# Performance work log

Measured on AMD Instinct MI355X. Metric: run time of the kernel, lower is better.

Reference implementation:

```python
import jax, jax.numpy as jnp
import numpy as np

# Problem sizes: batch B, n variables, m constraints (dense nnz pattern)
B, N, M = 256, 128, 192
# OSQP ADMM parameters (scaling=0, fixed rho; OSQP defaults)
RHO = 0.1      # step size
SIGMA = 1e-6   # regularization
ALPHA = 1.6    # relaxation
N_ITERS = 400  # fixed iteration count (jit-friendly surrogate for max_iter/tolerances)


def setup_inputs() -> dict:
    key = jax.random.key(0)
    k1, k2, k3, k4, k5, k6 = jax.random.split(key, 6)
    G = jax.random.normal(k1, (B, N, N), dtype=jnp.float32)
    # PSD quadratic cost: P = G G^T / n + 0.5 I
    P_val = jnp.einsum('bij,bkj->bik', G, G) / N + 0.5 * jnp.eye(N, dtype=jnp.float32)
    q_val = jax.random.normal(k2, (B, N), dtype=jnp.float32)
    A_val = jax.random.normal(k3, (B, M, N), dtype=jnp.float32) / jnp.sqrt(jnp.float32(N))
    # Bounds bracketing a feasible point x0 so every QP is solvable
    x0 = jax.random.normal(k4, (B, N), dtype=jnp.float32)
    z0 = jnp.einsum('bmn,bn->bm', A_val, x0)
    l_val = z0 - jnp.abs(jax.random.normal(k5, (B, M), dtype=jnp.float32)) - 0.1
    u_val = z0 + jnp.abs(jax.random.normal(k6, (B, M), dtype=jnp.float32)) + 0.1
    return {'P_val': P_val, 'q_val': q_val, 'A_val': A_val,
            'l_val': l_val, 'u_val': u_val}


def _osqp_admm(P, q, A, l, u):
    """Batched OSQP ADMM with fixed rho: solves argmin 1/2 x'Px + q'x s.t. l<=Ax<=u."""
    dt = P.dtype
    I_n = jnp.eye(N, dtype=dt)
    I_m = jnp.eye(M, dtype=dt)
    AT = jnp.swapaxes(A, -1, -2)  # [B, n, m]
    # KKT matrix [[P + sigma*I, A'], [A, -I/rho]]  -> [B, n+m, n+m]
    top = jnp.concatenate([P + SIGMA * I_n, AT], axis=-1)
    bot = jnp.concatenate([A, jnp.broadcast_to(-(1.0 / RHO) * I_m, (P.shape[0], M, M))], axis=-1)
    K = jnp.concatenate([top, bot], axis=-2)
    Kinv = jnp.linalg.inv(K)  # factorize once (rho fixed)

    x0 = jnp.zeros_like(q)
    z0 = jnp.zeros_like(l)
    y0 = jnp.zeros_like(l)

    def step(carry, _):
        x, z, y = carry
        rhs = jnp.concatenate([SIGMA * x - q, z - y / RHO], axis=-1)  # [B, n+m]
        sol = jnp.einsum('bij,bj->bi', Kinv, rhs)
        xt, nu = sol[:, :N], sol[:, N:]
        zt = z + (nu - y) / RHO
        x_new = ALPHA * xt + (1.0 - ALPHA) * x
        zc = ALPHA * zt + (1.0 - ALPHA) * z
        z_new = jnp.clip(zc + y / RHO, l, u)  # projection onto [l, u]
        y_new = y + RHO * (zc - z_new)
        return (x_new, z_new, y_new), None

    (x, z, y), _ = jax.lax.scan(step, (x0, z0, y0), None, length=N_ITERS)
    return x


def reference(P_val, q_val, A_val, l_val, u_val):
    # Returns the batch of primal solutions x_hat, shape [B, n]
    return _osqp_admm(P_val, q_val, A_val, l_val, u_val)
```

## Files before the change

kernel.cpp:

```cpp
#include <hip/hip_runtime.h>


#define Nn 128
#define Mm 192
constexpr float RHO_    = 0.1f;
constexpr float RHOINV_ = 10.0f;
constexpr float SIGMA_  = 1e-6f;
constexpr float ALPHA_  = 1.6f;
constexpr int   NITERS_ = 400;

typedef float v2f __attribute__((ext_vector_type(2)));
typedef float v4f __attribute__((ext_vector_type(4)));

template<int CTRL>
__device__ __forceinline__ float dpp_add(float x) {
  int y = __builtin_amdgcn_update_dpp(__float_as_int(x), __float_as_int(x),
                                      CTRL, 0xF, 0xF, false);
  return x + __int_as_float(y);
}
__device__ __forceinline__ float red16(float x) {
  x = dpp_add<0x121>(x); x = dpp_add<0x122>(x);
  x = dpp_add<0x124>(x); x = dpp_add<0x128>(x);
  return x;
}

template<int K0>
__device__ __forceinline__ void gj_block(float rr[32], float* __restrict__ buf0,
                                         float* __restrict__ buf1,
                                         const int irow, const int qq) {
  const bool qsel = (qq == K0);
  #pragma unroll
  for (int kk = 0; kk < 32; kk++) {
    const int k = 32*K0 + kk;
    float* wb = ((kk & 1) == 0) ? buf0 : buf1;
    if (irow == k) {
      #pragma unroll
      for (int j4 = 0; j4 < 8; j4++)
        *(float4*)&wb[36*qq + 4*j4] = *(const float4*)&rr[4*j4];
    }
    __syncthreads();
    const float akk  = wb[36*K0 + kk];
    float pinv = __builtin_amdgcn_rcpf(akk);
    pinv = pinv + pinv*(1.0f - akk*pinv);
    constexpr int QP = K0 | (K0<<2) | (K0<<4) | (K0<<6);
    const int fi = __builtin_amdgcn_update_dpp(__float_as_int(rr[kk]),
                      __float_as_int(rr[kk]), QP, 0xF, 0xF, false);
    const float f = __int_as_float(fi);
    const bool piv = (irow == k);
    float gfac = f * pinv;
    gfac = piv ? (1.0f - pinv) : gfac;
    float rk[32];
    #pragma unroll
    for (int j4 = 0; j4 < 8; j4++)
      *(float4*)&rk[4*j4] = *(const float4*)&wb[36*qq + 4*j4];
    #pragma unroll
    for (int j = 0; j < 32; j++) rr[j] -= gfac * rk[j];
    const float pivfix = piv ? pinv : -gfac;
    if (qsel) rr[kk] = pivfix;
  }
}

__global__ void __launch_bounds__(512, 2)
precompute_kernel(const float* __restrict__ Pg, const float* __restrict__ qg,
                  const float* __restrict__ Ag, float* __restrict__ wsWt,
                  float* __restrict__ wsC)
{
  __shared__ float smem[16384];
  const int t = threadIdx.x;
  const int b = blockIdx.x;
  const float* __restrict__ Pb = Pg + (size_t)b*Nn*Nn;
  const float* __restrict__ qb = qg + (size_t)b*Nn;
  const float* __restrict__ Ab = Ag + (size_t)b*Mm*Nn;

  {
    const int ar = t & 31;
    const int bc = t >> 5;
    float acc[4][8];
    #pragma unroll
    for (int a=0;a<4;a++)
      #pragma unroll
      for (int j=0;j<8;j++) acc[a][j]=0.f;

    for (int c=0;c<6;c++) {
      __syncthreads();
      {
        const float4* src = (const float4*)(Ab + c*32*Nn);
        float4* dst = (float4*)smem;
        dst[t]     = src[t];
        dst[t+512] = src[t+512];
      }
      __syncthreads();
      #pragma unroll 2
      for (int m=0;m<32;m++) {
        const float4 ra  = *(const float4*)&smem[m*Nn + 4*ar];
        const float4 cb0 = *(const float4*)&smem[m*Nn + 8*bc];
        const float4 cb1 = *(const float4*)&smem[m*Nn + 8*bc + 4];
        const float rv[4] = {ra.x, ra.y, ra.z, ra.w};
        const float cv[8] = {cb0.x,cb0.y,cb0.z,cb0.w,cb1.x,cb1.y,cb1.z,cb1.w};
        #pragma unroll
        for (int a=0;a<4;a++)
          #pragma unroll
          for (int j=0;j<8;j++) acc[a][j] += rv[a]*cv[j];
      }
    }
    __syncthreads();
    #pragma unroll
    for (int a=0;a<4;a++) {
      const int i = 4*ar + a;
      #pragma unroll
      for (int j=0;j<8;j++) {
        const int jj = 8*bc + j;
        float v = Pb[i*Nn + jj] + RHO_*acc[a][j];
        if (i == jj) v += SIGMA_;
        smem[i*Nn + jj] = v;
      }
    }
    __syncthreads();
  }

  {
    const int irow = t >> 2;
    const int qq   = t & 3;
    float rr[32];
    #pragma unroll
    for (int j=0;j<32;j++) rr[j] = smem[irow*Nn + 32*qq + j];
    __syncthreads();
    float* buf0 = smem;
    float* buf1 = smem + 144;
    gj_block<0>(rr, buf0, buf1, irow, qq);
    gj_block<1>(rr, buf0, buf1, irow, qq);
    gj_block<2>(rr, buf0, buf1, irow, qq);
    gj_block<3>(rr, buf0, buf1, irow, qq);
    __syncthreads();
    #pragma unroll
    for (int j=0;j<32;j++) smem[irow*Nn + 32*qq + j] = rr[j];
  }
  __syncthreads();

  {
    const int jr = t & 63, kc = t >> 6;
    v2f acc[3][8];
    #pragma unroll
    for (int a=0;a<3;a++)
      #pragma unroll
      for (int p=0;p<8;p++) acc[a][p] = (v2f){0.f,0.f};

    for (int mi=0; mi<32; mi++) {
      const v4f a0 = *(const v4f*)&Ab[(jr      )*Nn + 4*mi];
      const v4f a1 = *(const v4f*)&Ab[(jr +  64)*Nn + 4*mi];
      const v4f a2 = *(const v4f*)&Ab[(jr + 128)*Nn + 4*mi];
      const float am[3][4] = {{a0.x,a0.y,a0.z,a0.w},
                              {a1.x,a1.y,a1.z,a1.w},
                              {a2.x,a2.y,a2.z,a2.w}};
      #pragma unroll
      for (int q=0;q<4;q++) {
        const int m = 4*mi + q;
        const v4f w0 = *(const v4f*)&smem[m*Nn + 16*kc +  0];
        const v4f w1 = *(const v4f*)&smem[m*Nn + 16*kc +  4];
        const v4f w2 = *(const v4f*)&smem[m*Nn + 16*kc +  8];
        const v4f w3 = *(const v4f*)&smem[m*Nn + 16*kc + 12];
        const v2f wp[8] = {(v2f){w0.x,w0.y},(v2f){w0.z,w0.w},
                           (v2f){w1.x,w1.y},(v2f){w1.z,w1.w},
                           (v2f){w2.x,w2.y},(v2f){w2.z,w2.w},
                           (v2f){w3.x,w3.y},(v2f){w3.z,w3.w}};
        #pragma unroll
        for (int a=0;a<3;a++) {
          const v2f amv = (v2f){am[a][q], am[a][q]};
          #pragma unroll
          for (int p=0;p<8;p++) acc[a][p] += amv * wp[p];
        }
      }
    }
    float* wb = wsWt + (size_t)b*Mm*Nn;
    #pragma unroll
    for (int a=0;a<3;a++) {
      const int j = jr + 64*a;
      #pragma unroll
      for (int x=0;x<4;x++) {
        *(float4*)&wb[j*Nn + 16*kc + 4*x] =
          make_float4(acc[a][2*x].x, acc[a][2*x].y, acc[a][2*x+1].x, acc[a][2*x+1].y);
      }
    }
  }
  if (t < Nn) {
    float cc = 0.f;
    #pragma unroll 4
    for (int k=0;k<Nn;k++) cc += smem[k*Nn + t] * qb[k];
    wsC[(size_t)b*Nn + t] = cc;
  }
}

#define ABASE 0
#define WBASE 6912
__global__ void __launch_bounds__(1024, 4)
loop_kernel(const float* __restrict__ Ag, const float* __restrict__ lg,
            const float* __restrict__ ug, const float* __restrict__ wsWt,
            const float* __restrict__ wsC, float* __restrict__ outg)
{
  __shared__ float smem[13824];
  const int t = threadIdx.x, b = blockIdx.x;
  const int ig = t >> 4, cg = t & 15;
  const float* __restrict__ Ab = Ag   + (size_t)b*Mm*Nn;
  const float* __restrict__ Wb = wsWt + (size_t)b*Mm*Nn;
  const float* __restrict__ cb = wsC  + (size_t)b*Nn;

  const int  pm  = 64*cg + ig;
  const bool isp = (cg < 3);

  float dreg = 0.f, lreg = 0.f, ureg = 0.f;
  if (isp) {
    lreg = lg[(size_t)b*Mm + pm];
    ureg = ug[(size_t)b*Mm + pm];
    const float4* ar = (const float4*)(Ab + pm*Nn);
    const float4* cr = (const float4*)cb;
    #pragma unroll 4
    for (int k4=0;k4<32;k4++) {
      const float4 av = ar[k4], cv = cr[k4];
      dreg += av.x*cv.x + av.y*cv.y + av.z*cv.z + av.w*cv.w;
    }
  }

  v2f accv[3][12];
  #pragma unroll
  for (int a=0;a<3;a++)
    #pragma unroll
    for (int jj=0;jj<12;jj++) accv[a][jj] = (v2f){0.f,0.f};

  for (int kc=0; kc<4; kc++) {
    __syncthreads();
    {
      int x = t;
      {
        const int row = x>>3, c4 = x&7;
        *(float4*)&smem[ABASE + 36*row + 4*c4] = *(const float4*)&Ab[row*Nn + 32*kc + 4*c4];
        *(float4*)&smem[WBASE + 36*row + 4*c4] = *(const float4*)&Wb[row*Nn + 32*kc + 4*c4];
      }
      if (t < 512) {
        x = t + 1024;
        const int row = x>>3, c4 = x&7;
        *(float4*)&smem[ABASE + 36*row + 4*c4] = *(const float4*)&Ab[row*Nn + 32*kc + 4*c4];
        *(float4*)&smem[WBASE + 36*row + 4*c4] = *(const float4*)&Wb[row*Nn + 32*kc + 4*c4];
      }
    }
    __syncthreads();
    #pragma unroll
    for (int m4=0; m4<8; m4++) {
      const v4f a0 = *(const v4f*)&smem[ABASE + 36*(ig      ) + 4*m4];
      const v4f a1 = *(const v4f*)&smem[ABASE + 36*(ig +  64) + 4*m4];
      const v4f a2 = *(const v4f*)&smem[ABASE + 36*(ig + 128) + 4*m4];
      #pragma unroll
      for (int jj=0; jj<12; jj++) {
        const v4f w = *(const v4f*)&smem[WBASE + 36*(cg + 16*jj) + 4*m4];
        const v2f wlo = (v2f){w.x,w.y}, whi = (v2f){w.z,w.w};
        accv[0][jj] += (v2f){a0.x,a0.y}*wlo + (v2f){a0.z,a0.w}*whi;
        accv[1][jj] += (v2f){a1.x,a1.y}*wlo + (v2f){a1.z,a1.w}*whi;
        accv[2][jj] += (v2f){a2.x,a2.y}*wlo + (v2f){a2.z,a2.w}*whi;
      }
    }
  }
  float Vr[3][12];
  #pragma unroll
  for (int a=0;a<3;a++)
    #pragma unroll
    for (int jj=0;jj<12;jj++)
      Vr[a][jj] = accv[a][jj].x + accv[a][jj].y;

  __syncthreads();
  float* sT0  = smem;
  float* sT1  = smem + 192;
  float* sacc = smem + 384;
  if (t < Mm) sT0[t] = 0.f;
  __syncthreads();

  const int woff = (pm & 15)*12 + (pm >> 4);
  float sreg = 0.f, preg = 0.f, Sacc = 0.f;
  const float* sR0 = sT0 + 12*cg;
  const float* sR1 = sT1 + 12*cg;

#define ITER(RD, WR)                                                           \
  {                                                                            \
    const float4 sA = *(const float4*)(RD);                                    \
    const float4 sB = *(const float4*)((RD) + 4);                              \
    const float4 sC = *(const float4*)((RD) + 8);                              \
    float r0 = Vr[0][0]*sA.x + Vr[0][1]*sA.y + Vr[0][2]*sA.z + Vr[0][3]*sA.w   \
             + Vr[0][4]*sB.x + Vr[0][5]*sB.y + Vr[0][6]*sB.z + Vr[0][7]*sB.w   \
             + Vr[0][8]*sC.x + Vr[0][9]*sC.y + Vr[0][10]*sC.z + Vr[0][11]*sC.w;\
    float r1 = Vr[1][0]*sA.x + Vr[1][1]*sA.y + Vr[1][2]*sA.z + Vr[1][3]*sA.w   \
             + Vr[1][4]*sB.x + Vr[1][5]*sB.y + Vr[1][6]*sB.z + Vr[1][7]*sB.w   \
             + Vr[1][8]*sC.x + Vr[1][9]*sC.y + Vr[1][10]*sC.z + Vr[1][11]*sC.w;\
    float r2 = Vr[2][0]*sA.x + Vr[2][1]*sA.y + Vr[2][2]*sA.z + Vr[2][3]*sA.w   \
             + Vr[2][4]*sB.x + Vr[2][5]*sB.y + Vr[2][6]*sB.z + Vr[2][7]*sB.w   \
             + Vr[2][8]*sC.x + Vr[2][9]*sC.y + Vr[2][10]*sC.z + Vr[2][11]*sC.w;\
    r0 = red16(r0); r1 = red16(r1); r2 = red16(r2);                            \
    if (isp) {                                                                 \
      const float r  = (cg==0) ? r0 : ((cg==1) ? r1 : r2);                     \
      const float w  = r - dreg;                                               \
      const float v  = fmaf(ALPHA_, w, preg);                                  \
      const float z  = __builtin_amdgcn_fmed3f(v, lreg, ureg);                 \
      const float sn = RHO_ * fmaf(2.0f, z, -v);                               \
      (WR)[woff] = sn;                                                         \
      Sacc = (1.f-ALPHA_)*Sacc + ALPHA_*sreg;                                  \
      sreg = sn;                                                               \
      preg = fmaf(-ALPHA_, z, v);                                              \
    }                                                                          \
    __syncthreads();                                                           \
  }

  #pragma unroll 1
  for (int it2 = 0; it2 < NITERS_/2; it2++) {
    ITER(sR0, sT1)
    ITER(sR1, sT0)
  }
#undef ITER

  if (isp) sacc[pm] = Sacc;
  __syncthreads();
  if (t < Nn) {
    float acc = -cb[t];
    #pragma unroll 4
    for (int j=0;j<Mm;j++) acc += Wb[j*Nn + t] * sacc[j];
    outg[(size_t)b*Nn + t] = acc;
  }
}

extern "C" void kernel_launch(void* const* d_in, const int* in_sizes, int n_in,
                              void* d_out, int out_size, void* d_ws, size_t ws_size,
                              hipStream_t stream) {
  const float* P = (const float*)d_in[0];
  const float* q = (const float*)d_in[1];
  const float* A = (const float*)d_in[2];
  const float* l = (const float*)d_in[3];
  const float* u = (const float*)d_in[4];
  (void)in_sizes; (void)n_in; (void)out_size; (void)ws_size;
  float* wsWt = (float*)d_ws;
  float* wsC  = wsWt + (size_t)256*Mm*Nn;
  precompute_kernel<<<256, 512, 0, stream>>>(P, q, A, wsWt, wsC);
  loop_kernel<<<256, 1024, 0, stream>>>(A, l, u, wsWt, wsC, (float*)d_out);
}
```

Before: 461.2 us.

## Restructure ADMM loop to one thread per constraint with early exit

The loop kernel drops from 1024 to 256 threads per block. Each constraint thread now keeps its full 192-entry row of the iteration matrix in registers, which removes the 16-lane DPP reductions. W is stored transposed and staged in padded LDS, and the final x reconstruction reads from LDS. A fixed-point check every few iterations breaks out of the loop once the state stops changing bit-exactly, skipping the remaining iterations. The risks are heavy register pressure (192 floats per thread, one wave per EU) and a large dynamic LDS allocation.

After: 670.3 us. 1.45x slower.

```diff
diff --git a/kernel.cpp b/kernel.cpp
--- a/kernel.cpp
+++ b/kernel.cpp
@@ -4,25 +4,12 @@
 #define Nn 128
 #define Mm 192
 constexpr float RHO_    = 0.1f;
-constexpr float RHOINV_ = 10.0f;
 constexpr float SIGMA_  = 1e-6f;
 constexpr float ALPHA_  = 1.6f;
 constexpr int   NITERS_ = 400;
 
 typedef float v2f __attribute__((ext_vector_type(2)));
 typedef float v4f __attribute__((ext_vector_type(4)));
-
-template<int CTRL>
-__device__ __forceinline__ float dpp_add(float x) {
-  int y = __builtin_amdgcn_update_dpp(__float_as_int(x), __float_as_int(x),
-                                      CTRL, 0xF, 0xF, false);
-  return x + __int_as_float(y);
-}
-__device__ __forceinline__ float red16(float x) {
-  x = dpp_add<0x121>(x); x = dpp_add<0x122>(x);
-  x = dpp_add<0x124>(x); x = dpp_add<0x128>(x);
-  return x;
-}
 
 template<int K0>
 __device__ __forceinline__ void gj_block(float rr[32], float* __restrict__ buf0,
@@ -171,14 +158,15 @@
         }
       }
     }
-    float* wb = wsWt + (size_t)b*Mm*Nn;
+    float* wb = wsWt + (size_t)b*Nn*Mm;
     #pragma unroll
     for (int a=0;a<3;a++) {
       const int j = jr + 64*a;
       #pragma unroll
-      for (int x=0;x<4;x++) {
-        *(float4*)&wb[j*Nn + 16*kc + 4*x] =
-          make_float4(acc[a][2*x].x, acc[a][2*x].y, acc[a][2*x+1].x, acc[a][2*x+1].y);
+      for (int p=0;p<8;p++) {
+        const int col = 16*kc + 2*p;
+        wb[(size_t)(col    )*Mm + j] = acc[a][p].x;
+        wb[(size_t)(col + 1)*Mm + j] = acc[a][p].y;
       }
     }
   }
@@ -190,136 +178,134 @@
   }
 }
 
-#define ABASE 0
-#define WBASE 6912
-__global__ void __launch_bounds__(1024, 4)
+#define WT_LD 196
+#define OFF_S0   (Nn*WT_LD)
+#define OFF_S1   (OFF_S0 + Mm)
+#define OFF_SACC (OFF_S1 + Mm)
+#define OFF_C    (OFF_SACC + Mm)
+#define OFF_FLAG (OFF_C + Nn)
+#define LOOP_LDS_FLOATS (OFF_FLAG + 2)
+
+__global__ void __launch_bounds__(256)
+__attribute__((amdgpu_waves_per_eu(1, 1)))
 loop_kernel(const float* __restrict__ Ag, const float* __restrict__ lg,
-            const float* __restrict__ ug, const float* __restrict__ wsWt,
+            const float* __restrict__ ug, const float* __restrict__ wsWtT,
             const float* __restrict__ wsC, float* __restrict__ outg)
 {
-  __shared__ float smem[13824];
+  extern __shared__ float smem[];
   const int t = threadIdx.x, b = blockIdx.x;
-  const int ig = t >> 4, cg = t & 15;
+  const bool act = (t < Mm);
+  const float* __restrict__ Wg = wsWtT + (size_t)b*Nn*Mm;
+  const float* __restrict__ cb = wsC  + (size_t)b*Nn;
   const float* __restrict__ Ab = Ag   + (size_t)b*Mm*Nn;
-  const float* __restrict__ Wb = wsWt + (size_t)b*Mm*Nn;
-  const float* __restrict__ cb = wsC  + (size_t)b*Nn;
-
-  const int  pm  = 64*cg + ig;
-  const bool isp = (cg < 3);
+
+  float* WT    = smem;
+  float* sT0   = smem + OFF_S0;
+  float* sT1   = smem + OFF_S1;
+  float* sacc  = smem + OFF_SACC;
+  float* c_s   = smem + OFF_C;
+  float* sflag = smem + OFF_FLAG;
+
+  if (act) {
+    #pragma unroll 4
+    for (int k = 0; k < Nn; k++) WT[k*WT_LD + t] = Wg[(size_t)k*Mm + t];
+  }
+  if (t < Nn) c_s[t] = cb[t];
+  if (act) sT0[t] = 0.f;
+  if (t < 2) sflag[t] = 0.f;
+  __syncthreads();
 
   float dreg = 0.f, lreg = 0.f, ureg = 0.f;
-  if (isp) {
-    lreg = lg[(size_t)b*Mm + pm];
-    ureg = ug[(size_t)b*Mm + pm];
-    const float4* ar = (const float4*)(Ab + pm*Nn);
-    const float4* cr = (const float4*)cb;
+  v2f Vrow[96];
+  if (act) {
+    lreg = lg[(size_t)b*Mm + t];
+    ureg = ug[(size_t)b*Mm + t];
+    const float4* ar = (const float4*)(Ab + (size_t)t*Nn);
+    const float4* cr = (const float4*)c_s;
     #pragma unroll 4
-    for (int k4=0;k4<32;k4++) {
+    for (int k4 = 0; k4 < 32; k4++) {
       const float4 av = ar[k4], cv = cr[k4];
       dreg += av.x*cv.x + av.y*cv.y + av.z*cv.z + av.w*cv.w;
     }
-  }
-
-  v2f accv[3][12];
-  #pragma unroll
-  for (int a=0;a<3;a++)
-    #pragma unroll
-    for (int jj=0;jj<12;jj++) accv[a][jj] = (v2f){0.f,0.f};
-
-  for (int kc=0; kc<4; kc++) {
-    __syncthreads();
-    {
-      int x = t;
-      {
-        const int row = x>>3, c4 = x&7;
-        *(float4*)&smem[ABASE + 36*row + 4*c4] = *(const float4*)&Ab[row*Nn + 32*kc + 4*c4];
-        *(float4*)&smem[WBASE + 36*row + 4*c4] = *(const float4*)&Wb[row*Nn + 32*kc + 4*c4];
-      }
-      if (t < 512) {
-        x = t + 1024;
-        const int row = x>>3, c4 = x&7;
-        *(float4*)&smem[ABASE + 36*row + 4*c4] = *(const float4*)&Ab[row*Nn + 32*kc + 4*c4];
-        *(float4*)&smem[WBASE + 36*row + 4*c4] = *(const float4*)&Wb[row*Nn + 32*kc + 4*c4];
-      }
-    }
-    __syncthreads();
-    #pragma unroll
-    for (int m4=0; m4<8; m4++) {
-      const v4f a0 = *(const v4f*)&smem[ABASE + 36*(ig      ) + 4*m4];
-      const v4f a1 = *(const v4f*)&smem[ABASE + 36*(ig +  64) + 4*m4];
-      const v4f a2 = *(const v4f*)&smem[ABASE + 36*(ig + 128) + 4*m4];
-      #pragma unroll
-      for (int jj=0; jj<12; jj++) {
-        const v4f w = *(const v4f*)&smem[WBASE + 36*(cg + 16*jj) + 4*m4];
-        const v2f wlo = (v2f){w.x,w.y}, whi = (v2f){w.z,w.w};
-        accv[0][jj] += (v2f){a0.x,a0.y}*wlo + (v2f){a0.z,a0.w}*whi;
-        accv[1][jj] += (v2f){a1.x,a1.y}*wlo + (v2f){a1.z,a1.w}*whi;
-        accv[2][jj] += (v2f){a2.x,a2.y}*wlo + (v2f){a2.z,a2.w}*whi;
-      }
-    }
-  }
-  float Vr[3][12];
-  #pragma unroll
-  for (int a=0;a<3;a++)
-    #pragma unroll
-    for (int jj=0;jj<12;jj++)
-      Vr[a][jj] = accv[a][jj].x + accv[a][jj].y;
-
-  __syncthreads();
-  float* sT0  = smem;
-  float* sT1  = smem + 192;
-  float* sacc = smem + 384;
-  if (t < Mm) sT0[t] = 0.f;
-  __syncthreads();
-
-  const int woff = (pm & 15)*12 + (pm >> 4);
+    #pragma unroll
+    for (int p = 0; p < 96; p++) Vrow[p] = (v2f){0.f, 0.f};
+    for (int k2 = 0; k2 < 64; k2++) {
+      const v2f a2 = *(const v2f*)&Ab[(size_t)t*Nn + 2*k2];
+      const float* w0 = &WT[(2*k2    )*WT_LD];
+      const float* w1 = &WT[(2*k2 + 1)*WT_LD];
+      const v2f ax = (v2f){a2.x, a2.x};
+      const v2f ay = (v2f){a2.y, a2.y};
+      #pragma unroll
+      for (int p4 = 0; p4 < 48; p4++) {
+        const v4f wa = *(const v4f*)&w0[4*p4];
+        const v4f wv = *(const v4f*)&w1[4*p4];
+        Vrow[2*p4]   = __builtin_elementwise_fma(ax, (v2f){wa.x,wa.y}, Vrow[2*p4]);
+        Vrow[2*p4+1] = __builtin_elementwise_fma(ax, (v2f){wa.z,wa.w}, Vrow[2*p4+1]);
+        Vrow[2*p4]   = __builtin_elementwise_fma(ay, (v2f){wv.x,wv.y}, Vrow[2*p4]);
+        Vrow[2*p4+1] = __builtin_elementwise_fma(ay, (v2f){wv.z,wv.w}, Vrow[2*p4+1]);
+      }
+    }
+  }
+
   float sreg = 0.f, preg = 0.f, Sacc = 0.f;
-  const float* sR0 = sT0 + 12*cg;
-  const float* sR1 = sT1 + 12*cg;
-
-#define ITER(RD, WR)                                                           \
+  bool cvg = false;
+
+#define ITER(RD, WR, CHK, PH)                                                  \
   {                                                                            \
-    const float4 sA = *(const float4*)(RD);                                    \
-    const float4 sB = *(const float4*)((RD) + 4);                              \
-    const float4 sC = *(const float4*)((RD) + 8);                              \
-    float r0 = Vr[0][0]*sA.x + Vr[0][1]*sA.y + Vr[0][2]*sA.z + Vr[0][3]*sA.w   \
-             + Vr[0][4]*sB.x + Vr[0][5]*sB.y + Vr[0][6]*sB.z + Vr[0][7]*sB.w   \
-             + Vr[0][8]*sC.x + Vr[0][9]*sC.y + Vr[0][10]*sC.z + Vr[0][11]*sC.w;\
-    float r1 = Vr[1][0]*sA.x + Vr[1][1]*sA.y + Vr[1][2]*sA.z + Vr[1][3]*sA.w   \
-             + Vr[1][4]*sB.x + Vr[1][5]*sB.y + Vr[1][6]*sB.z + Vr[1][7]*sB.w   \
-             + Vr[1][8]*sC.x + Vr[1][9]*sC.y + Vr[1][10]*sC.z + Vr[1][11]*sC.w;\
-    float r2 = Vr[2][0]*sA.x + Vr[2][1]*sA.y + Vr[2][2]*sA.z + Vr[2][3]*sA.w   \
-             + Vr[2][4]*sB.x + Vr[2][5]*sB.y + Vr[2][6]*sB.z + Vr[2][7]*sB.w   \
-             + Vr[2][8]*sC.x + Vr[2][9]*sC.y + Vr[2][10]*sC.z + Vr[2][11]*sC.w;\
-    r0 = red16(r0); r1 = red16(r1); r2 = red16(r2);                            \
-    if (isp) {                                                                 \
-      const float r  = (cg==0) ? r0 : ((cg==1) ? r1 : r2);                     \
+    if (act) {                                                                 \
+      v2f q0 = (v2f){0.f,0.f}, q1 = (v2f){0.f,0.f};                            \
+      v2f q2 = (v2f){0.f,0.f}, q3 = (v2f){0.f,0.f};                            \
+      _Pragma("unroll")                                                        \
+      for (int p4 = 0; p4 < 24; p4++) {                                        \
+        const v4f sv = *(const v4f*)&(RD)[4*p4];                               \
+        const v4f sw = *(const v4f*)&(RD)[4*p4 + 96];                          \
+        q0 = __builtin_elementwise_fma(Vrow[2*p4],    (v2f){sv.x,sv.y}, q0);   \
+        q1 = __builtin_elementwise_fma(Vrow[2*p4+1],  (v2f){sv.z,sv.w}, q1);   \
+        q2 = __builtin_elementwise_fma(Vrow[2*p4+48], (v2f){sw.x,sw.y}, q2);   \
+        q3 = __builtin_elementwise_fma(Vrow[2*p4+49], (v2f){sw.z,sw.w}, q3);   \
+      }                                                                        \
+      q0 += q1; q2 += q3; q0 += q2;                                            \
+      const float r  = q0.x + q0.y;                                            \
       const float w  = r - dreg;                                               \
       const float v  = fmaf(ALPHA_, w, preg);                                  \
       const float z  = __builtin_amdgcn_fmed3f(v, lreg, ureg);                 \
       const float sn = RHO_ * fmaf(2.0f, z, -v);                               \
-      (WR)[woff] = sn;                                                         \
-      Sacc = (1.f-ALPHA_)*Sacc + ALPHA_*sreg;                                  \
-      sreg = sn;                                                               \
-      preg = fmaf(-ALPHA_, z, v);                                              \
+      const float pn = fmaf(-ALPHA_, z, v);                                    \
+      (WR)[t] = sn;                                                            \
+      if (CHK) { if (!(sn == sreg && pn == preg)) sflag[PH] = 1.f; }           \
+      Sacc = fmaf(1.0f - ALPHA_, Sacc, ALPHA_ * sreg);                         \
+      sreg = sn; preg = pn;                                                    \
     }                                                                          \
+    if ((CHK) && t == 0) sflag[(PH) ^ 1] = 0.f;                                \
     __syncthreads();                                                           \
+    if (CHK) cvg = (sflag[PH] == 0.f);                                         \
   }
 
   #pragma unroll 1
   for (int it2 = 0; it2 < NITERS_/2; it2++) {
-    ITER(sR0, sT1)
-    ITER(sR1, sT0)
+    ITER(sT0, sT1, false, 0)
+    const bool chk = ((it2 & 3) == 3) && (it2 < NITERS_/2 - 40);
+    const int ph = (it2 >> 2) & 1;
+    ITER(sT1, sT0, chk, ph)
+    if (cvg) break;
   }
 #undef ITER
-
-  if (isp) sacc[pm] = Sacc;
+  if (cvg && act) Sacc = sreg;
+
+  if (act) sacc[t] = Sacc;
   __syncthreads();
   if (t < Nn) {
-    float acc = -cb[t];
-    #pragma unroll 4
-    for (int j=0;j<Mm;j++) acc += Wb[j*Nn + t] * sacc[j];
-    outg[(size_t)b*Nn + t] = acc;
+    const float* wr = &WT[t*WT_LD];
+    v2f xa = (v2f){0.f,0.f}, xb = (v2f){0.f,0.f};
+    #pragma unroll
+    for (int j4 = 0; j4 < 48; j4++) {
+      const v4f wv = *(const v4f*)&wr[4*j4];
+      const v4f sv = *(const v4f*)&sacc[4*j4];
+      xa = __builtin_elementwise_fma((v2f){wv.x,wv.y}, (v2f){sv.x,sv.y}, xa);
+      xb = __builtin_elementwise_fma((v2f){wv.z,wv.w}, (v2f){sv.z,sv.w}, xb);
+    }
+    xa += xb;
+    outg[(size_t)b*Nn + t] = xa.x + xa.y - c_s[t];
   }
 }
 
@@ -335,5 +321,5 @@
   float* wsWt = (float*)d_ws;
   float* wsC  = wsWt + (size_t)256*Mm*Nn;
   precompute_kernel<<<256, 512, 0, stream>>>(P, q, A, wsWt, wsC);
-  loop_kernel<<<256, 1024, 0, stream>>>(A, l, u, wsWt, wsC, (float*)d_out);
+  loop_kernel<<<256, 256, LOOP_LDS_FLOATS*4, stream>>>(A, l, u, wsWt, wsC, (float*)d_out);
 }
```
